# Kernel optimization log

Measured on AMD Instinct MI355X. Metric: run time of the kernel, lower is better.

The kernel has to match this reference:

```python
import jax, jax.numpy as jnp
import numpy as np
from jax import lax

K_SIZE = 3
PAD = 1  # kernel // 2
BN_EPS = 1e-5


def _bilinear_gather(x, ys, xs):
    # x: [N,C,H,W]; ys, xs: [N,K,H,W] float sample coords -> [N,C,K,H,W]
    N, C, H, W = x.shape
    y0 = jnp.floor(ys)
    x0 = jnp.floor(xs)
    wy1 = ys - y0
    wx1 = xs - x0
    x_flat = x.reshape(N, C, H * W)

    def corner(yi, xi, wgt):
        valid = (yi >= 0) & (yi < H) & (xi >= 0) & (xi < W)
        yc = jnp.clip(yi, 0, H - 1).astype(jnp.int32)
        xc = jnp.clip(xi, 0, W - 1).astype(jnp.int32)
        idx = (yc * W + xc).reshape(N, -1)  # [N, K*H*W]
        g = jax.vmap(lambda xf, i: xf[:, i])(x_flat, idx)  # [N, C, K*H*W]
        g = g.reshape(N, C, ys.shape[1], H, W)
        return g * (wgt * valid.astype(x.dtype))[:, None]

    out = corner(y0, x0, (1 - wy1) * (1 - wx1))
    out = out + corner(y0, x0 + 1, (1 - wy1) * wx1)
    out = out + corner(y0 + 1, x0, wy1 * (1 - wx1))
    out = out + corner(y0 + 1, x0 + 1, wy1 * wx1)
    return out


def _dab_forward(x, w_off, b_off, w, b, gamma, beta):
    N, C, H, W = x.shape
    k = K_SIZE
    K = k * k
    # offset conv: 3x3, pad 1 -> [N, 2K, H, W]; per-tap (dy, dx) pairs
    offset = lax.conv_general_dilated(x, w_off, (1, 1), [(1, 1), (1, 1)])
    offset = offset + b_off[None, :, None, None]
    off = offset.reshape(N, K, 2, H, W)
    ky, kx = jnp.meshgrid(jnp.arange(k), jnp.arange(k), indexing='ij')
    base_y = (ky.reshape(K, 1, 1) + jnp.arange(H).reshape(1, H, 1) - PAD).astype(x.dtype)
    base_x = (kx.reshape(K, 1, 1) + jnp.arange(W).reshape(1, 1, W) - PAD).astype(x.dtype)
    ys = base_y[None] + off[:, :, 0]  # [N,K,H,W]
    xs = base_x[None] + off[:, :, 1]
    val = _bilinear_gather(x, ys, xs)  # [N,C,K,H,W]
    out = jnp.einsum('nckhw,ock->nohw', val, w.reshape(C, C, K))
    out = out + b[None, :, None, None]
    # BatchNorm2d (training-mode batch statistics, biased variance)
    mean = out.mean(axis=(0, 2, 3), keepdims=True)
    var = out.var(axis=(0, 2, 3), keepdims=True)
    out = (out - mean) * lax.rsqrt(var + BN_EPS)
    return out * gamma[None, :, None, None] + beta[None, :, None, None]


def setup_inputs() -> dict:
    key = jax.random.key(0)
    ks = jax.random.split(key, 6)
    N, C, H, W = 8, 64, 128, 128
    k = K_SIZE
    x = jax.random.normal(ks[0], (N, C, H, W), jnp.float32)
    w_off = jax.random.normal(ks[1], (2 * k * k, C, 3, 3), jnp.float32) * 0.02
    b_off = jax.random.normal(ks[2], (2 * k * k,), jnp.float32) * 0.02
    w = jax.random.normal(ks[3], (C, C, k, k), jnp.float32) * (1.0 / np.sqrt(C * k * k))
    b = jax.random.normal(ks[4], (C,), jnp.float32) * 0.02
    gamma = jnp.ones((C,), jnp.float32)
    beta = jnp.zeros((C,), jnp.float32)
    return {"x": x, "w_off": w_off, "b_off": b_off, "w": w, "b": b, "gamma": gamma, "beta": beta}


def reference(x, w_off, b_off, w, b, gamma, beta):
    return _dab_forward(x, w_off, b_off, w, b, gamma, beta)
```

## Files before the change

kernel.cpp:

```cpp
#include <hip/hip_runtime.h>
#include <hip/hip_bf16.h>

#define H 128
#define W 128
#define C 64
#define NB 8

typedef __attribute__((ext_vector_type(4))) float f32x4;
typedef __attribute__((ext_vector_type(8))) short short8;

static constexpr size_t XT_B  = 0;
static constexpr size_t CD_B  = 16777216;
static constexpr size_t WT_B  = 26214400;
static constexpr size_t WO_B  = 26288128;
static constexpr size_t SUM_B = 26324992;

__device__ __forceinline__ ushort f2bf(float f) {
  uint u = __float_as_uint(f);
  return (ushort)((u + 0x7fffu + ((u >> 16) & 1u)) >> 16);
}

union PackBF { __hip_bfloat162 h[4]; short8 s; };

#define UNPACK_FMA(q, wgt, m)                                  \
  m[0] += (wgt) * __uint_as_float((q).x << 16);                \
  m[1] += (wgt) * __uint_as_float((q).x & 0xffff0000u);        \
  m[2] += (wgt) * __uint_as_float((q).y << 16);                \
  m[3] += (wgt) * __uint_as_float((q).y & 0xffff0000u);        \
  m[4] += (wgt) * __uint_as_float((q).z << 16);                \
  m[5] += (wgt) * __uint_as_float((q).z & 0xffff0000u);        \
  m[6] += (wgt) * __uint_as_float((q).w << 16);                \
  m[7] += (wgt) * __uint_as_float((q).w & 0xffff0000u);

__global__ __launch_bounds__(256) void prep_kernel(const float* __restrict__ x,
                                                   const float* __restrict__ w,
                                                   const float* __restrict__ w_off,
                                                   ushort* __restrict__ xt,
                                                   ushort* __restrict__ wt,
                                                   ushort* __restrict__ wo,
                                                   float* __restrict__ sums) {
  int b = blockIdx.x, t = threadIdx.x;
  if (b < 1024) {
    __shared__ float lds[64 * 129];
    int n = b >> 7, h = b & 127;
    const float* xp = x + ((size_t)n * C) * H * W + (size_t)h * W;
    for (int i = t; i < 8192; i += 256) {
      int c = i >> 7, ww = i & 127;
      lds[c * 129 + ww] = xp[(size_t)c * H * W + ww];
    }
    __syncthreads();
    ushort* xo = xt + (((size_t)n * H + h) * W) * C;
    for (int i = t; i < 8192; i += 256) {
      int ww = i >> 6, c = i & 63;
      xo[(size_t)ww * C + c] = f2bf(lds[c * 129 + ww]);
    }
  } else if (b < 1040) {
    int base = (b - 1024) * 2304;
    for (int i = t; i < 2304; i += 256) {
      int idx = base + i;
      int k = idx >> 12;
      int r = idx & 4095;
      int ct = r >> 10, ln = (r >> 4) & 63, j = r & 15;
      int co = ct * 16 + (ln & 15);
      int c = ((ln >> 4) << 3) + (j < 8 ? j : 24 + j);
      wt[idx] = f2bf(w[co * 576 + c * 9 + k]);
    }
  } else if (b < 1048) {
    int base = (b - 1040) * 2304;
    for (int i = t; i < 2304; i += 256) {
      int idx = base + i;
      if (idx < 18432) {
        int k = idx >> 11;
        int r = idx & 2047;
        int f = r >> 9, ln = (r >> 3) & 63, j = r & 7;
        int o = ((f >> 1) << 4) + (ln & 15);
        int c = ((ln >> 4) << 3) + ((f & 1) << 5) + j;
        wo[idx] = (o < 18) ? f2bf(w_off[(o * 64 + c) * 9 + k]) : (ushort)0;
      }
    }
  } else {
    sums[t] = 0.0f;
    sums[t + 256] = 0.0f;
  }
}

__global__ __launch_bounds__(256, 4) void offs_kernel(const ushort* __restrict__ xt,
                                                      const ushort* __restrict__ wo,
                                                      const float* __restrict__ b_off,
                                                      float2* __restrict__ cd) {
  int b = blockIdx.x;
  int n = b & 7;
  int tile = b >> 3;
  int ty0 = (tile >> 4) << 3;
  int tx0 = (tile & 15) << 3;
  int t = threadIdx.x;
  int wv = t >> 6, ln = t & 63;
  int lr = ln & 15, lg = ln >> 4;
  int mypos = wv * 16 + lr;
  int ph = ty0 + (mypos >> 3), pw = tx0 + (mypos & 7);
  const ushort* xtn = xt + ((size_t)n << 20);

  __shared__ ushort xwin[256 * 64];

  {
    int by = ty0 - 4, bx = tx0 - 4;
#pragma unroll
    for (int i = 0; i < 8; ++i) {
      int chunk = i * 256 + t;
      int texel = chunk >> 3, slot = chunk & 7;
      int ry = texel >> 4, rx = texel & 15;
      int gy = min(max(by + ry, 0), H - 1);
      int gx = min(max(bx + rx, 0), W - 1);
      *(uint4*)&xwin[(texel << 6) + ((slot ^ (rx & 7)) << 3)] =
          *(const uint4*)(xtn + ((uint)((gy << 7) + gx) << 6) + (slot << 3));
    }
  }
  __syncthreads();

  f32x4 acc0 = {0.f, 0.f, 0.f, 0.f}, acc1 = {0.f, 0.f, 0.f, 0.f};
#pragma unroll
  for (int k = 0; k < 9; ++k) {
    int ky = k / 3 - 1, kx = k % 3 - 1;
    int gy = ph + ky, gx = pw + kx;
    bool v = (gy >= 0) & (gy < H) & (gx >= 0) & (gx < W);
    uint msk = v ? 0xffffffffu : 0u;
    int wry = (mypos >> 3) + 4 + ky, wrx = (mypos & 7) + 4 + kx;
    int texel = (wry << 4) + wrx;
    uint4 a = *(const uint4*)&xwin[(texel << 6) + ((lg ^ (wrx & 7)) << 3)];
    uint4 bq = *(const uint4*)&xwin[(texel << 6) + (((lg + 4) ^ (wrx & 7)) << 3)];
    a.x &= msk; a.y &= msk; a.z &= msk; a.w &= msk;
    bq.x &= msk; bq.y &= msk; bq.z &= msk; bq.w &= msk;
    short8 sa = *(short8*)&a, sb = *(short8*)&bq;
    const ushort* wk = wo + (((k << 2)) << 9) + (ln << 3);
    short8 b00 = *(const short8*)(wk);
    short8 b01 = *(const short8*)(wk + 512);
    short8 b10 = *(const short8*)(wk + 1024);
    short8 b11 = *(const short8*)(wk + 1536);
    acc0 = __builtin_amdgcn_mfma_f32_16x16x32_bf16(sa, b00, acc0, 0, 0, 0);
    acc0 = __builtin_amdgcn_mfma_f32_16x16x32_bf16(sb, b01, acc0, 0, 0, 0);
    acc1 = __builtin_amdgcn_mfma_f32_16x16x32_bf16(sa, b10, acc1, 0, 0, 0);
    acc1 = __builtin_amdgcn_mfma_f32_16x16x32_bf16(sb, b11, acc1, 0, 0, 0);
  }
  float bo0 = b_off[lr];
  float bo1 = (lr < 2) ? b_off[16 + lr] : 0.f;
  int rh[4], rw[4];
#pragma unroll
  for (int r = 0; r < 4; ++r) {
    int pos = wv * 16 + lg * 4 + r;
    rh[r] = ty0 + (pos >> 3);
    rw[r] = tx0 + (pos & 7);
  }
  float v0[4], p0[4], v1[4], p1[4];
#pragma unroll
  for (int r = 0; r < 4; ++r) { v0[r] = acc0[r] + bo0; v1[r] = acc1[r] + bo1; }
#pragma unroll
  for (int r = 0; r < 4; ++r) { p0[r] = __shfl_xor(v0[r], 1); p1[r] = __shfl_xor(v1[r], 1); }
  if (!(lr & 1)) {
    int k = lr >> 1;
    int ky = k / 3 - 1, kx = k % 3 - 1;
    float2* cdn = cd + (((size_t)n * 9 + k) << 14);
#pragma unroll
    for (int r = 0; r < 4; ++r)
      cdn[(rh[r] << 7) + rw[r]] = make_float2((float)(rh[r] + ky) + v0[r],
                                              (float)(rw[r] + kx) + p0[r]);
    if (lr == 0) {
      float2* cd8 = cd + (((size_t)n * 9 + 8) << 14);
#pragma unroll
      for (int r = 0; r < 4; ++r)
        cd8[(rh[r] << 7) + rw[r]] = make_float2((float)(rh[r] + 1) + v1[r],
                                                (float)(rw[r] + 1) + p1[r]);
    }
  }
}

__global__ __launch_bounds__(256, 4) void conv_kernel(const ushort* __restrict__ xt,
                                                      const float2* __restrict__ cd,
                                                      const ushort* __restrict__ wt,
                                                      const float* __restrict__ bias,
                                                      float* __restrict__ out,
                                                      float* __restrict__ sums) {
  int b = blockIdx.x;
  int n = b & 7;
  int tile = b >> 3;
  int ty0 = (tile >> 4) << 3;
  int tx0 = (tile & 15) << 3;
  int t = threadIdx.x;
  int wv = t >> 6, ln = t & 63;
  int lr = ln & 15, lg = ln >> 4;
  int mypos = wv * 16 + lr;
  int ph = ty0 + (mypos >> 3), pw = tx0 + (mypos & 7);
  int cb = lg << 3;
  int by = ty0 - 4, bx = tx0 - 4;

  __shared__ ushort xwin[256 * 64];
  __shared__ float red[4][64][2];

  const ushort* xtn = xt + ((size_t)n << 20);
  const float2* cdn = cd + (((size_t)n * 9) << 14) + (ph << 7) + pw;

  float2 cd2[9];
#pragma unroll
  for (int k = 0; k < 9; ++k) cd2[k] = cdn[(size_t)k << 14];

#pragma unroll
  for (int i = 0; i < 8; ++i) {
    int chunk = i * 256 + t;
    int texel = chunk >> 3, slot = chunk & 7;
    int ry = texel >> 4, rx = texel & 15;
    int gy = min(max(by + ry, 0), H - 1);
    int gx = min(max(bx + rx, 0), W - 1);
    *(uint4*)&xwin[(texel << 6) + ((slot ^ (rx & 7)) << 3)] =
        *(const uint4*)(xtn + ((uint)((gy << 7) + gx) << 6) + (slot << 3));
  }
  __syncthreads();

  f32x4 acc[4];
#pragma unroll
  for (int ct = 0; ct < 4; ++ct) acc[ct] = (f32x4)(0.f);

#pragma unroll
  for (int k = 0; k < 9; ++k) {
    float ys = cd2[k].x, xs = cd2[k].y;
    float y0f = floorf(ys), x0f = floorf(xs);
    float wy = ys - y0f, wx = xs - x0f;
    int iy0 = (int)y0f, ix0 = (int)x0f;
    int iy1 = iy0 + 1, ix1 = ix0 + 1;
    bool y0v = (iy0 >= 0) & (iy0 < H);
    bool y1v = (iy1 >= 0) & (iy1 < H);
    bool x0v = (ix0 >= 0) & (ix0 < W);
    bool x1v = (ix1 >= 0) & (ix1 < W);
    int yc0 = min(max(iy0, 0), H - 1), yc1 = min(max(iy1, 0), H - 1);
    int xc0 = min(max(ix0, 0), W - 1), xc1 = min(max(ix1, 0), W - 1);
    float w00 = (1.f - wy) * (1.f - wx) * (float)(y0v & x0v);
    float w01 = (1.f - wy) * wx * (float)(y0v & x1v);
    float w10 = wy * (1.f - wx) * (float)(y1v & x0v);
    float w11 = wy * wx * (float)(y1v & x1v);

    float m0[8] = {0.f, 0.f, 0.f, 0.f, 0.f, 0.f, 0.f, 0.f};
    float m1[8] = {0.f, 0.f, 0.f, 0.f, 0.f, 0.f, 0.f, 0.f};

#define CORNER(yc, xc, wgt) {                                                   \
    int ry_ = (yc) - by, rx_ = (xc) - bx;                                       \
    int ryc_ = min(max(ry_, 0), 15), rxc_ = min(max(rx_, 0), 15);               \
    int tex_ = (ryc_ << 4) + rxc_;                                              \
    uint4 qa_ = *(const uint4*)&xwin[(tex_ << 6) + ((lg ^ (rxc_ & 7)) << 3)];   \
    uint4 qb_ = *(const uint4*)&xwin[(tex_ << 6) + (((lg + 4) ^ (rxc_ & 7)) << 3)]; \
    if (__builtin_expect((((uint)ry_ >= 16u) | ((uint)rx_ >= 16u)) && (wgt) != 0.f, 0)) { \
      uint p_ = (uint)(((yc) << 7) + (xc)) << 6;                                \
      qa_ = *(const uint4*)(xtn + p_ + cb);                                     \
      qb_ = *(const uint4*)(xtn + p_ + cb + 32);                                \
    }                                                                           \
    UNPACK_FMA(qa_, wgt, m0); UNPACK_FMA(qb_, wgt, m1);                         \
  }

    CORNER(yc0, xc0, w00);
    CORNER(yc0, xc1, w01);
    CORNER(yc1, xc0, w10);
    CORNER(yc1, xc1, w11);
#undef CORNER

    PackBF a0, a1;
#pragma unroll
    for (int j = 0; j < 4; ++j) {
      a0.h[j] = __float22bfloat162_rn(make_float2(m0[2 * j], m0[2 * j + 1]));
      a1.h[j] = __float22bfloat162_rn(make_float2(m1[2 * j], m1[2 * j + 1]));
    }
    const ushort* wk = wt + (k << 12) + (ln << 4);
#pragma unroll
    for (int ct = 0; ct < 4; ++ct) {
      short8 b0 = *(const short8*)(wk + (ct << 10));
      short8 b1 = *(const short8*)(wk + (ct << 10) + 8);
      acc[ct] = __builtin_amdgcn_mfma_f32_16x16x32_bf16(a0.s, b0, acc[ct], 0, 0, 0);
      acc[ct] = __builtin_amdgcn_mfma_f32_16x16x32_bf16(a1.s, b1, acc[ct], 0, 0, 0);
    }
  }

  float bi[4];
#pragma unroll
  for (int ct = 0; ct < 4; ++ct) bi[ct] = bias[ct * 16 + lr];
  int phw[4];
#pragma unroll
  for (int r = 0; r < 4; ++r) {
    int pos = wv * 16 + lg * 4 + r;
    phw[r] = ((ty0 + (pos >> 3)) << 7) + tx0 + (pos & 7);
  }
  float s1[4], s2[4];
#pragma unroll
  for (int ct = 0; ct < 4; ++ct) { s1[ct] = 0.f; s2[ct] = 0.f; }
#pragma unroll
  for (int ct = 0; ct < 4; ++ct) {
    size_t cbase = ((size_t)(n * 64 + ct * 16 + lr)) << 14;
#pragma unroll
    for (int r = 0; r < 4; ++r) {
      float v = acc[ct][r] + bi[ct];
      out[cbase + phw[r]] = v;
      s1[ct] += v;
      s2[ct] += v * v;
    }
  }
#pragma unroll
  for (int ct = 0; ct < 4; ++ct) {
    s1[ct] += __shfl_xor(s1[ct], 16);
    s1[ct] += __shfl_xor(s1[ct], 32);
    s2[ct] += __shfl_xor(s2[ct], 16);
    s2[ct] += __shfl_xor(s2[ct], 32);
  }
  if (lg == 0) {
#pragma unroll
    for (int ct = 0; ct < 4; ++ct) {
      red[wv][ct * 16 + lr][0] = s1[ct];
      red[wv][ct * 16 + lr][1] = s2[ct];
    }
  }
  __syncthreads();
  if (t < 128) {
    int co = t & 63, j = t >> 6;
    float s = red[0][co][j] + red[1][co][j] + red[2][co][j] + red[3][co][j];
    atomicAdd(&sums[(b & 3) * 128 + j * 64 + co], s);
  }
}

__global__ __launch_bounds__(256) void bn_kernel(float* __restrict__ out,
                                                 const float* __restrict__ sums,
                                                 const float* __restrict__ gamma,
                                                 const float* __restrict__ beta) {
  size_t i4 = (size_t)blockIdx.x * 256 + threadIdx.x;
  size_t e = i4 * 4;
  int co = (int)((e >> 14) & 63);
  float s1 = sums[co] + sums[128 + co] + sums[256 + co] + sums[384 + co];
  float s2 = sums[64 + co] + sums[192 + co] + sums[320 + co] + sums[448 + co];
  const float inv_n = 1.f / 131072.f;
  float mean = s1 * inv_n;
  float var = s2 * inv_n - mean * mean;
  float iv = rsqrtf(var + 1e-5f);
  float sc = gamma[co] * iv;
  float sh = beta[co] - mean * sc;
  float4 v = ((float4*)out)[i4];
  v.x = v.x * sc + sh;
  v.y = v.y * sc + sh;
  v.z = v.z * sc + sh;
  v.w = v.w * sc + sh;
  ((float4*)out)[i4] = v;
}

extern "C" void kernel_launch(void* const* d_in, const int* in_sizes, int n_in,
                              void* d_out, int out_size, void* d_ws, size_t ws_size,
                              hipStream_t stream) {
  (void)in_sizes; (void)n_in; (void)out_size; (void)ws_size;
  const float* x     = (const float*)d_in[0];
  const float* w_off = (const float*)d_in[1];
  const float* b_off = (const float*)d_in[2];
  const float* w     = (const float*)d_in[3];
  const float* bias  = (const float*)d_in[4];
  const float* gamma = (const float*)d_in[5];
  const float* beta  = (const float*)d_in[6];
  uint8_t* wsb = (uint8_t*)d_ws;
  ushort* xtp  = (ushort*)(wsb + XT_B);
  float2* cdp  = (float2*)(wsb + CD_B);
  ushort* wtp  = (ushort*)(wsb + WT_B);
  ushort* wop  = (ushort*)(wsb + WO_B);
  float* sums  = (float*)(wsb + SUM_B);
  float* out   = (float*)d_out;

  hipLaunchKernelGGL(prep_kernel, dim3(1049), dim3(256), 0, stream, x, w, w_off, xtp, wtp, wop, sums);
  hipLaunchKernelGGL(offs_kernel, dim3(2048), dim3(256), 0, stream, xtp, wop, b_off, cdp);
  hipLaunchKernelGGL(conv_kernel, dim3(2048), dim3(256), 0, stream, xtp, cdp, wtp, bias, out, sums);
  hipLaunchKernelGGL(bn_kernel, dim3(8192), dim3(256), 0, stream, out, sums, gamma, beta);
}
```

Baseline: 168.5 us.

## Switch to fp16 storage, packed half FMA bilinear blend, and fp16 pre-BN buffer

Stores x and the weights as fp16 instead of bf16 and uses f16 MFMA. The bilinear corner blend now runs with packed __hfma2, which removes the per-element unpack-to-float FMAs and the repacking step. The conv output before BatchNorm is written as fp16 into a workspace buffer, then bn_kernel reads it and writes fp32, which halves the intermediate traffic. The risk is lower accuracy: fp16 accumulation of the blend, and fp16 rounding of outputs before the statistics are applied, though the sums themselves are still computed in fp32.

```diff
diff --git a/kernel.cpp b/kernel.cpp
--- a/kernel.cpp
+++ b/kernel.cpp
@@ -1,5 +1,5 @@
 #include <hip/hip_runtime.h>
-#include <hip/hip_bf16.h>
+#include <hip/hip_fp16.h>
 
 #define H 128
 #define W 128
@@ -7,30 +7,23 @@
 #define NB 8
 
 typedef __attribute__((ext_vector_type(4))) float f32x4;
-typedef __attribute__((ext_vector_type(8))) short short8;
+typedef __attribute__((ext_vector_type(8))) _Float16 f16x8;
 
 static constexpr size_t XT_B  = 0;
 static constexpr size_t CD_B  = 16777216;
 static constexpr size_t WT_B  = 26214400;
 static constexpr size_t WO_B  = 26288128;
 static constexpr size_t SUM_B = 26324992;
-
-__device__ __forceinline__ ushort f2bf(float f) {
-  uint u = __float_as_uint(f);
-  return (ushort)((u + 0x7fffu + ((u >> 16) & 1u)) >> 16);
-}
-
-union PackBF { __hip_bfloat162 h[4]; short8 s; };
-
-#define UNPACK_FMA(q, wgt, m)                                  \
-  m[0] += (wgt) * __uint_as_float((q).x << 16);                \
-  m[1] += (wgt) * __uint_as_float((q).x & 0xffff0000u);        \
-  m[2] += (wgt) * __uint_as_float((q).y << 16);                \
-  m[3] += (wgt) * __uint_as_float((q).y & 0xffff0000u);        \
-  m[4] += (wgt) * __uint_as_float((q).z << 16);                \
-  m[5] += (wgt) * __uint_as_float((q).z & 0xffff0000u);        \
-  m[6] += (wgt) * __uint_as_float((q).w << 16);                \
-  m[7] += (wgt) * __uint_as_float((q).w & 0xffff0000u);
+static constexpr size_t PB_B  = 26327040;
+
+__device__ __forceinline__ ushort f2h(float f) {
+  __half h = __float2half_rn(f);
+  return *reinterpret_cast<ushort*>(&h);
+}
+
+union QH  { uint4 q; f16x8 h; };
+union AH  { __half2 h[4]; f16x8 v; };
+union PK2 { __half2 h[2]; uint2 u; };
 
 __global__ __launch_bounds__(256) void prep_kernel(const float* __restrict__ x,
                                                    const float* __restrict__ w,
@@ -52,7 +45,7 @@
     ushort* xo = xt + (((size_t)n * H + h) * W) * C;
     for (int i = t; i < 8192; i += 256) {
       int ww = i >> 6, c = i & 63;
-      xo[(size_t)ww * C + c] = f2bf(lds[c * 129 + ww]);
+      xo[(size_t)ww * C + c] = f2h(lds[c * 129 + ww]);
     }
   } else if (b < 1040) {
     int base = (b - 1024) * 2304;
@@ -63,7 +56,7 @@
       int ct = r >> 10, ln = (r >> 4) & 63, j = r & 15;
       int co = ct * 16 + (ln & 15);
       int c = ((ln >> 4) << 3) + (j < 8 ? j : 24 + j);
-      wt[idx] = f2bf(w[co * 576 + c * 9 + k]);
+      wt[idx] = f2h(w[co * 576 + c * 9 + k]);
     }
   } else if (b < 1048) {
     int base = (b - 1040) * 2304;
@@ -75,7 +68,7 @@
         int f = r >> 9, ln = (r >> 3) & 63, j = r & 7;
         int o = ((f >> 1) << 4) + (ln & 15);
         int c = ((ln >> 4) << 3) + ((f & 1) << 5) + j;
-        wo[idx] = (o < 18) ? f2bf(w_off[(o * 64 + c) * 9 + k]) : (ushort)0;
+        wo[idx] = (o < 18) ? f2h(w_off[(o * 64 + c) * 9 + k]) : (ushort)0;
       }
     }
   } else {
@@ -126,20 +119,20 @@
     uint msk = v ? 0xffffffffu : 0u;
     int wry = (mypos >> 3) + 4 + ky, wrx = (mypos & 7) + 4 + kx;
     int texel = (wry << 4) + wrx;
-    uint4 a = *(const uint4*)&xwin[(texel << 6) + ((lg ^ (wrx & 7)) << 3)];
-    uint4 bq = *(const uint4*)&xwin[(texel << 6) + (((lg + 4) ^ (wrx & 7)) << 3)];
-    a.x &= msk; a.y &= msk; a.z &= msk; a.w &= msk;
-    bq.x &= msk; bq.y &= msk; bq.z &= msk; bq.w &= msk;
-    short8 sa = *(short8*)&a, sb = *(short8*)&bq;
-    const ushort* wk = wo + (((k << 2)) << 9) + (ln << 3);
-    short8 b00 = *(const short8*)(wk);
-    short8 b01 = *(const short8*)(wk + 512);
-    short8 b10 = *(const short8*)(wk + 1024);
-    short8 b11 = *(const short8*)(wk + 1536);
-    acc0 = __builtin_amdgcn_mfma_f32_16x16x32_bf16(sa, b00, acc0, 0, 0, 0);
-    acc0 = __builtin_amdgcn_mfma_f32_16x16x32_bf16(sb, b01, acc0, 0, 0, 0);
-    acc1 = __builtin_amdgcn_mfma_f32_16x16x32_bf16(sa, b10, acc1, 0, 0, 0);
-    acc1 = __builtin_amdgcn_mfma_f32_16x16x32_bf16(sb, b11, acc1, 0, 0, 0);
+    QH qa, qb;
+    qa.q = *(const uint4*)&xwin[(texel << 6) + ((lg ^ (wrx & 7)) << 3)];
+    qb.q = *(const uint4*)&xwin[(texel << 6) + (((lg + 4) ^ (wrx & 7)) << 3)];
+    qa.q.x &= msk; qa.q.y &= msk; qa.q.z &= msk; qa.q.w &= msk;
+    qb.q.x &= msk; qb.q.y &= msk; qb.q.z &= msk; qb.q.w &= msk;
+    const ushort* wk = wo + (k << 11) + (ln << 3);
+    f16x8 b00 = *(const f16x8*)(const void*)(wk);
+    f16x8 b01 = *(const f16x8*)(const void*)(wk + 512);
+    f16x8 b10 = *(const f16x8*)(const void*)(wk + 1024);
+    f16x8 b11 = *(const f16x8*)(const void*)(wk + 1536);
+    acc0 = __builtin_amdgcn_mfma_f32_16x16x32_f16(qa.h, b00, acc0, 0, 0, 0);
+    acc0 = __builtin_amdgcn_mfma_f32_16x16x32_f16(qb.h, b01, acc0, 0, 0, 0);
+    acc1 = __builtin_amdgcn_mfma_f32_16x16x32_f16(qa.h, b10, acc1, 0, 0, 0);
+    acc1 = __builtin_amdgcn_mfma_f32_16x16x32_f16(qb.h, b11, acc1, 0, 0, 0);
   }
   float bo0 = b_off[lr];
   float bo1 = (lr < 2) ? b_off[16 + lr] : 0.f;
@@ -177,7 +170,7 @@
                                                       const float2* __restrict__ cd,
                                                       const ushort* __restrict__ wt,
                                                       const float* __restrict__ bias,
-                                                      float* __restrict__ out,
+                                                      ushort* __restrict__ pb,
                                                       float* __restrict__ sums) {
   int b = blockIdx.x;
   int n = b & 7;
@@ -217,6 +210,7 @@
   f32x4 acc[4];
 #pragma unroll
   for (int ct = 0; ct < 4; ++ct) acc[ct] = (f32x4)(0.f);
+  const __half2 HZ = __floats2half2_rn(0.f, 0.f);
 
 #pragma unroll
   for (int k = 0; k < 9; ++k) {
@@ -235,11 +229,14 @@
     float w01 = (1.f - wy) * wx * (float)(y0v & x1v);
     float w10 = wy * (1.f - wx) * (float)(y1v & x0v);
     float w11 = wy * wx * (float)(y1v & x1v);
-
-    float m0[8] = {0.f, 0.f, 0.f, 0.f, 0.f, 0.f, 0.f, 0.f};
-    float m1[8] = {0.f, 0.f, 0.f, 0.f, 0.f, 0.f, 0.f, 0.f};
-
-#define CORNER(yc, xc, wgt) {                                                   \
+    __half2 W00 = __float2half2_rn(w00), W01 = __float2half2_rn(w01);
+    __half2 W10 = __float2half2_rn(w10), W11 = __float2half2_rn(w11);
+
+    AH m0, m1;
+#pragma unroll
+    for (int j = 0; j < 4; ++j) { m0.h[j] = HZ; m1.h[j] = HZ; }
+
+#define CORNER(yc, xc, wgt, WW) {                                               \
     int ry_ = (yc) - by, rx_ = (xc) - bx;                                       \
     int ryc_ = min(max(ry_, 0), 15), rxc_ = min(max(rx_, 0), 15);               \
     int tex_ = (ryc_ << 4) + rxc_;                                              \
@@ -250,53 +247,53 @@
       qa_ = *(const uint4*)(xtn + p_ + cb);                                     \
       qb_ = *(const uint4*)(xtn + p_ + cb + 32);                                \
     }                                                                           \
-    UNPACK_FMA(qa_, wgt, m0); UNPACK_FMA(qb_, wgt, m1);                         \
-  }
-
-    CORNER(yc0, xc0, w00);
-    CORNER(yc0, xc1, w01);
-    CORNER(yc1, xc0, w10);
-    CORNER(yc1, xc1, w11);
+    const __half2* pa_ = (const __half2*)&qa_;                                  \
+    const __half2* pb_ = (const __half2*)&qb_;                                  \
+    m0.h[0] = __hfma2(WW, pa_[0], m0.h[0]);                                     \
+    m0.h[1] = __hfma2(WW, pa_[1], m0.h[1]);                                     \
+    m0.h[2] = __hfma2(WW, pa_[2], m0.h[2]);                                     \
+    m0.h[3] = __hfma2(WW, pa_[3], m0.h[3]);                                     \
+    m1.h[0] = __hfma2(WW, pb_[0], m1.h[0]);                                     \
+    m1.h[1] = __hfma2(WW, pb_[1], m1.h[1]);                                     \
+    m1.h[2] = __hfma2(WW, pb_[2], m1.h[2]);                                     \
+    m1.h[3] = __hfma2(WW, pb_[3], m1.h[3]);                                     \
+  }
+
+    CORNER(yc0, xc0, w00, W00);
+    CORNER(yc0, xc1, w01, W01);
+    CORNER(yc1, xc0, w10, W10);
+    CORNER(yc1, xc1, w11, W11);
 #undef CORNER
 
-    PackBF a0, a1;
-#pragma unroll
-    for (int j = 0; j < 4; ++j) {
-      a0.h[j] = __float22bfloat162_rn(make_float2(m0[2 * j], m0[2 * j + 1]));
-      a1.h[j] = __float22bfloat162_rn(make_float2(m1[2 * j], m1[2 * j + 1]));
-    }
     const ushort* wk = wt + (k << 12) + (ln << 4);
 #pragma unroll
     for (int ct = 0; ct < 4; ++ct) {
-      short8 b0 = *(const short8*)(wk + (ct << 10));
-      short8 b1 = *(const short8*)(wk + (ct << 10) + 8);
-      acc[ct] = __builtin_amdgcn_mfma_f32_16x16x32_bf16(a0.s, b0, acc[ct], 0, 0, 0);
-      acc[ct] = __builtin_amdgcn_mfma_f32_16x16x32_bf16(a1.s, b1, acc[ct], 0, 0, 0);
+      f16x8 b0 = *(const f16x8*)(const void*)(wk + (ct << 10));
+      f16x8 b1 = *(const f16x8*)(const void*)(wk + (ct << 10) + 8);
+      acc[ct] = __builtin_amdgcn_mfma_f32_16x16x32_f16(m0.v, b0, acc[ct], 0, 0, 0);
+      acc[ct] = __builtin_amdgcn_mfma_f32_16x16x32_f16(m1.v, b1, acc[ct], 0, 0, 0);
     }
   }
 
   float bi[4];
 #pragma unroll
   for (int ct = 0; ct < 4; ++ct) bi[ct] = bias[ct * 16 + lr];
-  int phw[4];
-#pragma unroll
-  for (int r = 0; r < 4; ++r) {
-    int pos = wv * 16 + lg * 4 + r;
-    phw[r] = ((ty0 + (pos >> 3)) << 7) + tx0 + (pos & 7);
-  }
+  int pos0 = wv * 16 + lg * 4;
+  int phw0 = ((ty0 + (pos0 >> 3)) << 7) + tx0 + (pos0 & 7);
   float s1[4], s2[4];
 #pragma unroll
-  for (int ct = 0; ct < 4; ++ct) { s1[ct] = 0.f; s2[ct] = 0.f; }
-#pragma unroll
   for (int ct = 0; ct < 4; ++ct) {
-    size_t cbase = ((size_t)(n * 64 + ct * 16 + lr)) << 14;
-#pragma unroll
-    for (int r = 0; r < 4; ++r) {
-      float v = acc[ct][r] + bi[ct];
-      out[cbase + phw[r]] = v;
-      s1[ct] += v;
-      s2[ct] += v * v;
-    }
+    float v0 = acc[ct][0] + bi[ct];
+    float v1 = acc[ct][1] + bi[ct];
+    float v2 = acc[ct][2] + bi[ct];
+    float v3 = acc[ct][3] + bi[ct];
+    size_t cbase = ((size_t)(n * 64 + ct * 16 + lr) << 14) + phw0;
+    PK2 pk;
+    pk.h[0] = __floats2half2_rn(v0, v1);
+    pk.h[1] = __floats2half2_rn(v2, v3);
+    *(uint2*)&pb[cbase] = pk.u;
+    s1[ct] = v0 + v1 + v2 + v3;
+    s2[ct] = v0 * v0 + v1 * v1 + v2 * v2 + v3 * v3;
   }
 #pragma unroll
   for (int ct = 0; ct < 4; ++ct) {
@@ -320,7 +317,8 @@
   }
 }
 
-__global__ __launch_bounds__(256) void bn_kernel(float* __restrict__ out,
+__global__ __launch_bounds__(256) void bn_kernel(const ushort* __restrict__ pb,
+                                                 float* __restrict__ out,
                                                  const float* __restrict__ sums,
                                                  const float* __restrict__ gamma,
                                                  const float* __restrict__ beta) {
@@ -335,12 +333,16 @@
   float iv = rsqrtf(var + 1e-5f);
   float sc = gamma[co] * iv;
   float sh = beta[co] - mean * sc;
-  float4 v = ((float4*)out)[i4];
-  v.x = v.x * sc + sh;
-  v.y = v.y * sc + sh;
-  v.z = v.z * sc + sh;
-  v.w = v.w * sc + sh;
-  ((float4*)out)[i4] = v;
+  PK2 q;
+  q.u = ((const uint2*)pb)[i4];
+  float2 f0 = __half22float2(q.h[0]);
+  float2 f1 = __half22float2(q.h[1]);
+  float4 o;
+  o.x = f0.x * sc + sh;
+  o.y = f0.y * sc + sh;
+  o.z = f1.x * sc + sh;
+  o.w = f1.y * sc + sh;
+  ((float4*)out)[i4] = o;
 }
 
 extern "C" void kernel_launch(void* const* d_in, const int* in_sizes, int n_in,
@@ -360,10 +362,11 @@
   ushort* wtp  = (ushort*)(wsb + WT_B);
   ushort* wop  = (ushort*)(wsb + WO_B);
   float* sums  = (float*)(wsb + SUM_B);
+  ushort* pbp  = (ushort*)(wsb + PB_B);
   float* out   = (float*)d_out;
 
   hipLaunchKernelGGL(prep_kernel, dim3(1049), dim3(256), 0, stream, x, w, w_off, xtp, wtp, wop, sums);
   hipLaunchKernelGGL(offs_kernel, dim3(2048), dim3(256), 0, stream, xtp, wop, b_off, cdp);
-  hipLaunchKernelGGL(conv_kernel, dim3(2048), dim3(256), 0, stream, xtp, cdp, wtp, bias, out, sums);
-  hipLaunchKernelGGL(bn_kernel, dim3(8192), dim3(256), 0, stream, out, sums, gamma, beta);
-}
+  hipLaunchKernelGGL(conv_kernel, dim3(2048), dim3(256), 0, stream, xtp, cdp, wtp, bias, pbp, sums);
+  hipLaunchKernelGGL(bn_kernel, dim3(8192), dim3(256), 0, stream, pbp, out, sums, gamma, beta);
+}
```

After: 163.9 us. 1.03x faster.
